# Optimization experiments

Hardware: AMD Instinct MI355X
Metric: run time of the kernel (lower is better)

## Reference

```python
import jax, jax.numpy as jnp
import numpy as np

B, N, C = 4, 4096, 64
ALPHA = 0.2        # leaky relu slope
THRESHOLD = 0.5    # adjacency threshold
NEG_INF = -9e15


def setup_inputs() -> dict:
    key = jax.random.key(0)
    k1, k2, k3 = jax.random.split(key, 3)
    inp = jax.random.normal(k1, (B, N, C), dtype=jnp.float32)
    adj = jax.random.uniform(k2, (N, N), dtype=jnp.float32)
    # xavier_uniform with gain=1.414 on shape (2C, 1)
    bound = 1.414 * float(np.sqrt(6.0 / (2 * C + 1)))
    a = jax.random.uniform(k3, (2 * C, 1), dtype=jnp.float32, minval=-bound, maxval=bound)
    return {"input": inp, "adj": adj, "a": a}


def reference(input, adj, a):
    h = input                          # [B, N, C]
    a1 = a[:C, 0]                      # scores from source node i
    a2 = a[C:, 0]                      # scores from target node j
    # e[b,i,j] = leakyrelu(a1.h_i + a2.h_j)  (avoids O(N^2 * 2C) concat)
    s1 = h @ a1                        # [B, N]
    s2 = h @ a2                        # [B, N]
    e = s1[:, :, None] + s2[:, None, :]
    e = jnp.where(e > 0, e, ALPHA * e)
    mask = adj[None, :, :] > THRESHOLD
    att = jnp.where(mask, e, NEG_INF)
    att = jax.nn.softmax(att, axis=2)  # [B, N, N]
    h_prime = jnp.einsum('bij,bjc->bic', att, h)
    return jax.nn.elu(h_prime)         # concat=True -> elu
```

## Files before the change

### kernel.cpp

```cpp
#include <hip/hip_runtime.h>
#include <hip/hip_bf16.h>

#define B_ 4
#define N_ 4096
#define C_ 64

constexpr float LOG2E = 1.44269504088896340736f;

typedef __attribute__((ext_vector_type(8))) short short8;
typedef __attribute__((ext_vector_type(4))) float f32x4;

#if __has_builtin(__builtin_amdgcn_exp2f)
#define EXP2F(x) __builtin_amdgcn_exp2f(x)
#else
#define EXP2F(x) exp2f(x)
#endif

static __device__ inline short f32_to_bf16_bits(float f) {
    union { __hip_bfloat16 h; unsigned short u; } cv;
    cv.h = __float2bfloat16(f);
    return (short)cv.u;
}

__global__ __launch_bounds__(256) void gat_prep(
    const float* __restrict__ h, const float* __restrict__ a,
    float* __restrict__ s1s, float* __restrict__ s2s,
    unsigned short* __restrict__ hT)
{
    const int bid = blockIdx.x;
    const int b = bid >> 6;
    const int i0 = (bid & 63) * 64;
    __shared__ float tile[64][65];
    const int t = threadIdx.x;
    {
        const int rr = t >> 2;
        const int cc = (t & 3) * 16;
        const float* src = h + ((size_t)(b * N_ + i0 + rr)) * C_ + cc;
        float d1 = 0.f, d2 = 0.f;
#pragma unroll
        for (int k = 0; k < 16; k += 4) {
            float4 v = *(const float4*)(src + k);
            tile[rr][cc + k + 0] = v.x;
            tile[rr][cc + k + 1] = v.y;
            tile[rr][cc + k + 2] = v.z;
            tile[rr][cc + k + 3] = v.w;
            float4 a1 = *(const float4*)(a + cc + k);
            float4 a2 = *(const float4*)(a + C_ + cc + k);
            d1 += v.x * a1.x + v.y * a1.y + v.z * a1.z + v.w * a1.w;
            d2 += v.x * a2.x + v.y * a2.y + v.z * a2.z + v.w * a2.w;
        }
        d1 += __shfl_xor(d1, 1, 64); d1 += __shfl_xor(d1, 2, 64);
        d2 += __shfl_xor(d2, 1, 64); d2 += __shfl_xor(d2, 2, 64);
        if ((t & 3) == 0) {
            s1s[b * N_ + i0 + rr] = d1 * LOG2E;
            s2s[b * N_ + i0 + rr] = d2 * LOG2E;
        }
    }
    __syncthreads();
    {
        const int c  = t >> 2;
        const int ic = (t & 3) * 16;
        short8 w0, w1;
#pragma unroll
        for (int k = 0; k < 8; ++k)
            w0[k] = f32_to_bf16_bits(tile[ic + k][c]);
#pragma unroll
        for (int k = 0; k < 8; ++k)
            w1[k] = f32_to_bf16_bits(tile[ic + 8 + k][c]);
        unsigned short* dst = hT + ((size_t)(b * C_ + c)) * N_ + i0 + ic;
        *(short8*)(dst)     = w0;
        *(short8*)(dst + 8) = w1;
    }
}

__global__ __launch_bounds__(256) void gat_main(
    const float* __restrict__ adj, const float* __restrict__ s1s,
    const float* __restrict__ s2s, const unsigned short* __restrict__ hT,
    float* __restrict__ accP, float* __restrict__ lP, int jsNum)
{
    const int bid  = blockIdx.x;
    const int itb  = bid / jsNum;
    const int js   = bid % jsNum;
    const int jlen = N_ / jsNum;
    const int j0   = js * jlen;
    const int i0   = itb * 32;
    const int lane = threadIdx.x & 63;
    const int b    = threadIdx.x >> 6;
    const int g    = lane >> 4;
    const int r16  = lane & 15;

    float s1v[2];
    s1v[0] = s1s[b * N_ + i0 + r16];
    s1v[1] = s1s[b * N_ + i0 + 16 + r16];

    f32x4 acc[2][4];
#pragma unroll
    for (int it = 0; it < 2; ++it)
#pragma unroll
        for (int ct = 0; ct < 4; ++ct)
            acc[it][ct] = (f32x4){0.f, 0.f, 0.f, 0.f};
    f32x4 accL[2];
    accL[0] = (f32x4){0.f, 0.f, 0.f, 0.f};
    accL[1] = (f32x4){0.f, 0.f, 0.f, 0.f};

    short8 ones;
#pragma unroll
    for (int q = 0; q < 8; ++q) ones[q] = (short)0x3F80;

    const unsigned short* hTb = hT + (size_t)b * C_ * N_;
    const float* s2b   = s2s + b * N_;
    const float* adjR0 = adj + (size_t)(i0 + r16) * N_;
    const float* adjR1 = adj + (size_t)(i0 + 16 + r16) * N_;
    const int kbase = j0 + g * 8;

    for (int jj = 0; jj < jlen; jj += 32) {
        const int kb = kbase + jj;

        short8 bfrag[4];
#pragma unroll
        for (int ct = 0; ct < 4; ++ct)
            bfrag[ct] = *(const short8*)(hTb + (size_t)(ct * 16 + r16) * N_ + kb);

        float4 sa = *(const float4*)(s2b + kb);
        float4 sb = *(const float4*)(s2b + kb + 4);
        float s2v[8] = {sa.x, sa.y, sa.z, sa.w, sb.x, sb.y, sb.z, sb.w};

        float4 a00 = *(const float4*)(adjR0 + kb);
        float4 a01 = *(const float4*)(adjR0 + kb + 4);
        float4 a10 = *(const float4*)(adjR1 + kb);
        float4 a11 = *(const float4*)(adjR1 + kb + 4);
        float adjv[2][8] = {
            {a00.x, a00.y, a00.z, a00.w, a01.x, a01.y, a01.z, a01.w},
            {a10.x, a10.y, a10.z, a10.w, a11.x, a11.y, a11.z, a11.w}};

#pragma unroll
        for (int it = 0; it < 2; ++it) {
            const float s1 = s1v[it];
            short8 afrag;
#pragma unroll
            for (int q = 0; q < 8; ++q) {
                float e = s1 + s2v[q];
                e = fmaxf(e, 0.2f * e);
                float p = (adjv[it][q] > 0.5f) ? EXP2F(e) : 0.0f;
                afrag[q] = f32_to_bf16_bits(p);
            }
#pragma unroll
            for (int ct = 0; ct < 4; ++ct)
                acc[it][ct] = __builtin_amdgcn_mfma_f32_16x16x32_bf16(
                    afrag, bfrag[ct], acc[it][ct], 0, 0, 0);
            accL[it] = __builtin_amdgcn_mfma_f32_16x16x32_bf16(
                afrag, ones, accL[it], 0, 0, 0);
        }
    }

    const size_t pb = (size_t)js * B_ + b;
    if (r16 == 0) {
#pragma unroll
        for (int it = 0; it < 2; ++it)
#pragma unroll
            for (int r = 0; r < 4; ++r)
                lP[pb * N_ + i0 + it * 16 + g * 4 + r] = accL[it][r];
    }

    float* accBase = accP + pb * (size_t)N_ * C_;
#pragma unroll
    for (int it = 0; it < 2; ++it)
#pragma unroll
        for (int ct = 0; ct < 4; ++ct)
#pragma unroll
            for (int r = 0; r < 4; ++r) {
                const int i = i0 + it * 16 + g * 4 + r;
                const int c = ct * 16 + r16;
                accBase[(size_t)i * C_ + c] = acc[it][ct][r];
            }
}

__global__ __launch_bounds__(256) void gat_combine(
    const float* __restrict__ accP, const float* __restrict__ lP,
    float* __restrict__ out, int jsNum)
{
    const int t = blockIdx.x * 256 + threadIdx.x;
    const int total4 = B_ * N_ * C_ / 4;
    if (t >= total4) return;
    const int bi = t >> 4;
    float4 asum = {0.f, 0.f, 0.f, 0.f};
    float lsum = 0.f;
    for (int p = 0; p < jsNum; ++p) {
        float4 v = ((const float4*)accP)[(size_t)p * total4 + t];
        asum.x += v.x; asum.y += v.y; asum.z += v.z; asum.w += v.w;
        lsum += lP[(size_t)p * (B_ * N_) + bi];
    }
    const float inv = 1.0f / lsum;
    float4 o;
    o.x = asum.x * inv; o.y = asum.y * inv; o.z = asum.z * inv; o.w = asum.w * inv;
    o.x = (o.x > 0.f) ? o.x : (expf(o.x) - 1.f);
    o.y = (o.y > 0.f) ? o.y : (expf(o.y) - 1.f);
    o.z = (o.z > 0.f) ? o.z : (expf(o.z) - 1.f);
    o.w = (o.w > 0.f) ? o.w : (expf(o.w) - 1.f);
    ((float4*)out)[t] = o;
}

extern "C" void kernel_launch(void* const* d_in, const int* in_sizes, int n_in,
                              void* d_out, int out_size, void* d_ws, size_t ws_size,
                              hipStream_t stream)
{
    const float* h   = (const float*)d_in[0];
    const float* adj = (const float*)d_in[1];
    const float* a   = (const float*)d_in[2];
    float* out = (float*)d_out;

    char* ws = (char*)d_ws;
    float* s1s = (float*)ws;
    float* s2s = (float*)(ws + (size_t)B_ * N_ * 4);
    unsigned short* hT = (unsigned short*)(ws + (size_t)2 * B_ * N_ * 4);
    const size_t lOff = (size_t)2 * B_ * N_ * 4 + (size_t)B_ * C_ * N_ * 2;

    int jsNum = 8;
    while (jsNum > 1) {
        size_t need = lOff + (size_t)jsNum * B_ * N_ * 4
                           + (size_t)jsNum * B_ * N_ * C_ * 4;
        if (need <= ws_size) break;
        jsNum >>= 1;
    }
    float* lP   = (float*)(ws + lOff);
    float* accP = (float*)(ws + lOff + (size_t)jsNum * B_ * N_ * 4);

    gat_prep<<<B_ * (N_ / 64), 256, 0, stream>>>(h, a, s1s, s2s, hT);
    gat_main<<<128 * jsNum, 256, 0, stream>>>(adj, s1s, s2s, hT, accP, lP, jsNum);
    gat_combine<<<(B_ * N_ * C_ / 4 + 255) / 256, 256, 0, stream>>>(accP, lP, out, jsNum);
}
```

Measured before the change: 167.8 us.

## Precompute adjacency threshold as transposed bitmask before attention kernel

Adds a kernel that thresholds the fp32 adjacency matrix into a packed 32-bit bitmask, stored transposed so that consecutive rows are contiguous per word column. The main attention kernel then reads one mask word per row per 32 columns instead of eight floats, which cuts its global load traffic and register use. The cost is an extra launch and a full extra pass over the adjacency matrix.

```diff
diff --git a/kernel.cpp b/kernel.cpp
--- a/kernel.cpp
+++ b/kernel.cpp
@@ -4,6 +4,7 @@
 #define B_ 4
 #define N_ 4096
 #define C_ 64
+#define NW_ (N_ / 32)
 
 constexpr float LOG2E = 1.44269504088896340736f;
 
@@ -73,8 +74,26 @@
     }
 }
 
+__global__ __launch_bounds__(256) void gat_mask(
+    const float* __restrict__ adj, unsigned int* __restrict__ maskT)
+{
+    const int wave = threadIdx.x >> 6;
+    const int lane = threadIdx.x & 63;
+    const int row = blockIdx.x * 4 + wave;
+    const float* arow = adj + (size_t)row * N_;
+#pragma unroll 4
+    for (int jw = 0; jw < N_ / 64; ++jw) {
+        float v = arow[jw * 64 + lane];
+        unsigned long long bal = __ballot(v > 0.5f);
+        if (lane == 0)
+            maskT[(size_t)(2 * jw) * N_ + row] = (unsigned int)bal;
+        else if (lane == 32)
+            maskT[(size_t)(2 * jw + 1) * N_ + row] = (unsigned int)(bal >> 32);
+    }
+}
+
 __global__ __launch_bounds__(256) void gat_main(
-    const float* __restrict__ adj, const float* __restrict__ s1s,
+    const unsigned int* __restrict__ maskT, const float* __restrict__ s1s,
     const float* __restrict__ s2s, const unsigned short* __restrict__ hT,
     float* __restrict__ accP, float* __restrict__ lP, int jsNum)
 {
@@ -108,13 +127,13 @@
     for (int q = 0; q < 8; ++q) ones[q] = (short)0x3F80;
 
     const unsigned short* hTb = hT + (size_t)b * C_ * N_;
-    const float* s2b   = s2s + b * N_;
-    const float* adjR0 = adj + (size_t)(i0 + r16) * N_;
-    const float* adjR1 = adj + (size_t)(i0 + 16 + r16) * N_;
+    const float* s2b = s2s + b * N_;
     const int kbase = j0 + g * 8;
+    const int gsh = g * 8;
 
     for (int jj = 0; jj < jlen; jj += 32) {
         const int kb = kbase + jj;
+        const int w = (j0 + jj) >> 5;
 
         short8 bfrag[4];
 #pragma unroll
@@ -125,23 +144,20 @@
         float4 sb = *(const float4*)(s2b + kb + 4);
         float s2v[8] = {sa.x, sa.y, sa.z, sa.w, sb.x, sb.y, sb.z, sb.w};
 
-        float4 a00 = *(const float4*)(adjR0 + kb);
-        float4 a01 = *(const float4*)(adjR0 + kb + 4);
-        float4 a10 = *(const float4*)(adjR1 + kb);
-        float4 a11 = *(const float4*)(adjR1 + kb + 4);
-        float adjv[2][8] = {
-            {a00.x, a00.y, a00.z, a00.w, a01.x, a01.y, a01.z, a01.w},
-            {a10.x, a10.y, a10.z, a10.w, a11.x, a11.y, a11.z, a11.w}};
+        const unsigned int* mw = maskT + (size_t)w * N_ + i0;
+        unsigned int m0 = mw[r16] >> gsh;
+        unsigned int m1 = mw[16 + r16] >> gsh;
 
 #pragma unroll
         for (int it = 0; it < 2; ++it) {
             const float s1 = s1v[it];
+            const unsigned int m = it ? m1 : m0;
             short8 afrag;
 #pragma unroll
             for (int q = 0; q < 8; ++q) {
                 float e = s1 + s2v[q];
                 e = fmaxf(e, 0.2f * e);
-                float p = (adjv[it][q] > 0.5f) ? EXP2F(e) : 0.0f;
+                float p = ((m >> q) & 1u) ? EXP2F(e) : 0.0f;
                 afrag[q] = f32_to_bf16_bits(p);
             }
 #pragma unroll
@@ -213,7 +229,9 @@
     float* s1s = (float*)ws;
     float* s2s = (float*)(ws + (size_t)B_ * N_ * 4);
     unsigned short* hT = (unsigned short*)(ws + (size_t)2 * B_ * N_ * 4);
-    const size_t lOff = (size_t)2 * B_ * N_ * 4 + (size_t)B_ * C_ * N_ * 2;
+    const size_t maskOff = (size_t)2 * B_ * N_ * 4 + (size_t)B_ * C_ * N_ * 2;
+    unsigned int* maskT = (unsigned int*)(ws + maskOff);
+    const size_t lOff = maskOff + (size_t)NW_ * N_ * 4;
 
     int jsNum = 8;
     while (jsNum > 1) {
@@ -226,6 +244,7 @@
     float* accP = (float*)(ws + lOff + (size_t)jsNum * B_ * N_ * 4);
 
     gat_prep<<<B_ * (N_ / 64), 256, 0, stream>>>(h, a, s1s, s2s, hT);
-    gat_main<<<128 * jsNum, 256, 0, stream>>>(adj, s1s, s2s, hT, accP, lP, jsNum);
+    gat_mask<<<N_ / 4, 256, 0, stream>>>(adj, maskT);
+    gat_main<<<128 * jsNum, 256, 0, stream>>>(maskT, s1s, s2s, hT, accP, lP, jsNum);
     gat_combine<<<(B_ * N_ * C_ / 4 + 255) / 256, 256, 0, stream>>>(accP, lP, out, jsNum);
 }
```

Result: slower. 180.4 us (+7.5%).
